# Performance work log

Measured on AMD Instinct MI355X. Metric: run time of the kernel, lower is better.

## Reference

```python
import jax, jax.numpy as jnp
import numpy as np

SPINS = (16, 16)
D_FEAT = 1024
H1 = (4096, 4096, 2048)
H2 = (2048, 1)


def _pair_idx(n):
    # Matches: idx_h1 = [i for i in range(n-1) for j in range(n-1-i)]
    #          h2 = concat(h[k:] for k in 1..n-1)  -> all ordered pairs (i, j), i < j
    i = np.repeat(np.arange(n - 1), np.arange(n - 1, 0, -1))
    j = np.concatenate([np.arange(k + 1, n) for k in range(n - 1)])
    return i.astype(np.int32), j.astype(np.int32)


def setup_inputs():
    key = jax.random.key(0)
    ks = jax.random.split(key, 6)

    def w(k, fi, fo, scale):
        return (scale / np.sqrt(fi)).astype(np.float32) * jax.random.normal(k, (fi, fo), jnp.float32)

    d_in = 2 * D_FEAT
    return {
        "h_one": jax.random.normal(ks[0], (sum(SPINS), D_FEAT), jnp.float32),
        "w1_0": w(ks[1], d_in, H1[0], np.float32(np.sqrt(2.0))),
        "b1_0": jnp.zeros((H1[0],), jnp.float32),
        "w1_1": w(ks[2], H1[0], H1[1], np.float32(np.sqrt(2.0))),
        "b1_1": jnp.zeros((H1[1],), jnp.float32),
        # final mlp1 layer scaled so |hidden| ~ 2: keeps the pair-product finite in fp32
        "w1_2": w(ks[3], H1[1], H1[2], np.float32(2.0)),
        "b1_2": jnp.zeros((H1[2],), jnp.float32),
        "w2_0": w(ks[4], H1[2], H2[0], np.float32(1.0)),
        "b2_0": jnp.zeros((H2[0],), jnp.float32),
        "w2_1": w(ks[5], H2[0], H2[1], np.float32(1.0)),
        "b2_1": jnp.zeros((H2[1],), jnp.float32),
    }


def reference(h_one, w1_0, b1_0, w1_1, b1_1, w1_2, b1_2, w2_0, b2_0, w2_1, b2_1):
    def mlp1(x):  # silu hidden layers, linear output
        x = jax.nn.silu(x @ w1_0 + b1_0)
        x = jax.nn.silu(x @ w1_1 + b1_1)
        return x @ w1_2 + b1_2

    def mlp2(x):  # tanh hidden layer, linear scalar output
        x = jnp.tanh(x @ w2_0 + b2_0)
        return x @ w2_1 + b2_1

    sumlogA = jnp.float32(0.0)
    off = 0
    for n in SPINS:  # fixed, small, structurally distinct loop over spin channels
        h = h_one[off:off + n]
        off += n
        ii, jj = _pair_idx(n)  # static numpy indices
        h1, h2 = h[ii], h[jj]  # [P, D] pairwise gathers, P = n*(n-1)/2
        hidden = mlp1(jnp.concatenate([h1, h2], axis=-1)) \
               - mlp1(jnp.concatenate([h2, h1], axis=-1))  # antisymmetric in (h1, h2)
        a = jnp.prod(hidden, axis=0)  # product-reduce over pairs -> [H1[-1]]
        A = mlp2(a)                   # [1]
        sumlogA = sumlogA + jnp.log(jnp.abs(A)).squeeze()
    return sumlogA
```

## Files before the change

### kernel.cpp

```cpp
#include <hip/hip_runtime.h>
#include <hip/hip_bf16.h>
#include <math.h>


typedef __attribute__((ext_vector_type(8))) short short8;
typedef __attribute__((ext_vector_type(4))) float floatx4;

#define AS1 __attribute__((address_space(1)))
#define AS3 __attribute__((address_space(3)))
#define GLD16(g, l) __builtin_amdgcn_global_load_lds((AS1 const unsigned int*)(g), (AS3 unsigned int*)(l), 16, 0, 0)

__device__ __forceinline__ float silu_f(float x) {
    return x / (1.0f + __expf(-x));
}

__device__ __forceinline__ void split2(float x, unsigned short& hi, unsigned short& lo) {
    unsigned u = __float_as_uint(x);
    unsigned r = u + 0x7FFFu + ((u >> 16) & 1u);
    unsigned short h = (unsigned short)(r >> 16);
    float hf = __uint_as_float((unsigned)h << 16);
    float rem = x - hf;
    unsigned u2 = __float_as_uint(rem);
    unsigned r2 = u2 + 0x7FFFu + ((u2 >> 16) & 1u);
    hi = h;
    lo = (unsigned short)(r2 >> 16);
}

__global__ __launch_bounds__(256)
void transpose_split_all(const float* __restrict__ w10, const float* __restrict__ w11,
                         const float* __restrict__ w12, const float* __restrict__ h_one,
                         unsigned short* __restrict__ t10h, unsigned short* __restrict__ t10l,
                         unsigned short* __restrict__ t11h, unsigned short* __restrict__ t11l,
                         unsigned short* __restrict__ t12h, unsigned short* __restrict__ t12l,
                         unsigned short* __restrict__ Hh, unsigned short* __restrict__ Hl) {
    const int t = threadIdx.x;
    int id = blockIdx.x;

    if (id >= 8192) {
        const int base = (id - 8192) * 4096 + t * 16;
        #pragma unroll
        for (int j = 0; j < 4; ++j) {
            float4 v = *(const float4*)&h_one[base + 4 * j];
            ushort4 hv, lv;
            split2(v.x, hv.x, lv.x);
            split2(v.y, hv.y, lv.y);
            split2(v.z, hv.z, lv.z);
            split2(v.w, hv.w, lv.w);
            *(ushort4*)&Hh[base + 4 * j] = hv;
            *(ushort4*)&Hl[base + 4 * j] = lv;
        }
        return;
    }

    const float* W;
    unsigned short *Th, *Tl;
    int K, N, nt, kt;
    if (id < 2048)       { W = w10; Th = t10h; Tl = t10l; K = 2048; N = 4096; nt = id & 63; kt = id >> 6; }
    else if (id < 6144)  { id -= 2048; W = w11; Th = t11h; Tl = t11l; K = 4096; N = 4096; nt = id & 63; kt = id >> 6; }
    else                 { id -= 6144; W = w12; Th = t12h; Tl = t12l; K = 4096; N = 2048; nt = id & 31; kt = id >> 5; }

    __shared__ float tile[64][65];
    const int n0 = nt * 64;
    const int k0 = kt * 64;

    const int lr = t >> 2;
    const int lc = (t & 3) * 16;
    const float* src = &W[(size_t)(k0 + lr) * N + n0 + lc];
    #pragma unroll
    for (int j = 0; j < 4; ++j) {
        float4 v = *(const float4*)(src + 4 * j);
        tile[lr][lc + 4 * j + 0] = v.x;
        tile[lr][lc + 4 * j + 1] = v.y;
        tile[lr][lc + 4 * j + 2] = v.z;
        tile[lr][lc + 4 * j + 3] = v.w;
    }
    __syncthreads();

    const int sn   = t >> 2;
    const int koff = (t & 3) * 16;
    unsigned short hv[16], lv[16];
    #pragma unroll
    for (int kk = 0; kk < 16; ++kk)
        split2(tile[koff + kk][sn], hv[kk], lv[kk]);
    unsigned short* dh = &Th[(size_t)(n0 + sn) * K + k0 + koff];
    unsigned short* dl = &Tl[(size_t)(n0 + sn) * K + k0 + koff];
    *(short8*)(dh)     = *(short8*)&hv[0];
    *(short8*)(dh + 8) = *(short8*)&hv[8];
    *(short8*)(dl)     = *(short8*)&lv[0];
    *(short8*)(dl + 8) = *(short8*)&lv[8];
}

__global__ __launch_bounds__(256, 2)
void gemm128(const unsigned short* __restrict__ Ah, const unsigned short* __restrict__ Al,
             const unsigned short* __restrict__ Bh, const unsigned short* __restrict__ Bl,
             int K, float* __restrict__ Cpart, int N, int Mtot, int kc)
{
    __shared__ __align__(16) unsigned short As[2][128][32];
    __shared__ __align__(16) unsigned short Bs[2][128][32];

    const int tid  = threadIdx.x;
    const int lane = tid & 63;
    const int wid  = tid >> 6;
    const int n0 = blockIdx.x * 128;
    const int m0 = blockIdx.y * 128;
    const int kbase = blockIdx.z * kc;

    const int srow   = wid * 32 + (lane >> 2);
    const int schunk = (lane & 3) ^ ((srow >> 1) & 3);
    const unsigned short* gA0h = Ah + (size_t)(m0 + srow) * K + kbase + schunk * 8;
    const unsigned short* gA1h = gA0h + (size_t)16 * K;
    const unsigned short* gA0l = Al + (size_t)(m0 + srow) * K + kbase + schunk * 8;
    const unsigned short* gA1l = gA0l + (size_t)16 * K;
    const unsigned short* gB0h = Bh + (size_t)(n0 + srow) * K + kbase + schunk * 8;
    const unsigned short* gB1h = gB0h + (size_t)16 * K;
    const unsigned short* gB0l = Bl + (size_t)(n0 + srow) * K + kbase + schunk * 8;
    const unsigned short* gB1l = gB0l + (size_t)16 * K;
    unsigned short* lA0h = &As[0][wid * 32][0];
    unsigned short* lA1h = &As[0][wid * 32 + 16][0];
    unsigned short* lA0l = &As[1][wid * 32][0];
    unsigned short* lA1l = &As[1][wid * 32 + 16][0];
    unsigned short* lB0h = &Bs[0][wid * 32][0];
    unsigned short* lB1h = &Bs[0][wid * 32 + 16][0];
    unsigned short* lB0l = &Bs[1][wid * 32][0];
    unsigned short* lB1l = &Bs[1][wid * 32 + 16][0];

    const int mhalf = wid >> 1;
    const int nhalf = wid & 1;
    const int lm = lane & 15;
    const int q  = lane >> 4;
    int aoffs[4], boffs[4];
    #pragma unroll
    for (int f = 0; f < 4; ++f) {
        int arow = mhalf * 64 + f * 16 + lm;
        int aslot = q ^ ((arow >> 1) & 3);
        aoffs[f] = arow * 32 + aslot * 8;
        int brow = nhalf * 64 + f * 16 + lm;
        int bslot = q ^ ((brow >> 1) & 3);
        boffs[f] = brow * 32 + bslot * 8;
    }
    const unsigned short* AsF = &As[0][0][0];
    const unsigned short* BsF = &Bs[0][0][0];

    floatx4 acc[4][4];
    #pragma unroll
    for (int ms = 0; ms < 4; ++ms)
        #pragma unroll
        for (int ns = 0; ns < 4; ++ns)
            acc[ms][ns] = (floatx4){0.f, 0.f, 0.f, 0.f};

    const int S = kc >> 5;
    for (int s = 0; s < S; ++s) {
        const int ko = s << 5;
        __syncthreads();
        GLD16(gA0h + ko, lA0h);
        GLD16(gA1h + ko, lA1h);
        GLD16(gA0l + ko, lA0l);
        GLD16(gA1l + ko, lA1l);
        GLD16(gB0h + ko, lB0h);
        GLD16(gB1h + ko, lB1h);
        GLD16(gB0l + ko, lB0l);
        GLD16(gB1l + ko, lB1l);
        __syncthreads();

        short8 afh[4], afl[4], bfh[4], bfl[4];
        #pragma unroll
        for (int f = 0; f < 4; ++f) {
            afh[f] = *(const short8*)(AsF + aoffs[f]);
            afl[f] = *(const short8*)(AsF + 4096 + aoffs[f]);
            bfh[f] = *(const short8*)(BsF + boffs[f]);
            bfl[f] = *(const short8*)(BsF + 4096 + boffs[f]);
        }
        #pragma unroll
        for (int ms = 0; ms < 4; ++ms)
            #pragma unroll
            for (int ns = 0; ns < 4; ++ns)
                acc[ms][ns] = __builtin_amdgcn_mfma_f32_16x16x32_bf16(afh[ms], bfh[ns], acc[ms][ns], 0, 0, 0);
        #pragma unroll
        for (int ms = 0; ms < 4; ++ms)
            #pragma unroll
            for (int ns = 0; ns < 4; ++ns)
                acc[ms][ns] = __builtin_amdgcn_mfma_f32_16x16x32_bf16(afl[ms], bfh[ns], acc[ms][ns], 0, 0, 0);
        #pragma unroll
        for (int ms = 0; ms < 4; ++ms)
            #pragma unroll
            for (int ns = 0; ns < 4; ++ns)
                acc[ms][ns] = __builtin_amdgcn_mfma_f32_16x16x32_bf16(afh[ms], bfl[ns], acc[ms][ns], 0, 0, 0);
    }

    float* Cp = Cpart + (size_t)blockIdx.z * Mtot * N;
    const int lr = (lane >> 4) * 4;
    #pragma unroll
    for (int ms = 0; ms < 4; ++ms)
        #pragma unroll
        for (int ns = 0; ns < 4; ++ns)
            #pragma unroll
            for (int r = 0; r < 4; ++r)
                Cp[(size_t)(m0 + mhalf * 64 + ms * 16 + lr + r) * N + n0 + nhalf * 64 + ns * 16 + lm] = acc[ms][ns][r];
}

__device__ __forceinline__ void load_set(
    const unsigned short* __restrict__ Ah, const unsigned short* __restrict__ Al,
    const unsigned short* __restrict__ Bh, const unsigned short* __restrict__ Bl,
    const unsigned aoff[4], const unsigned boff[4], int koff,
    short8 (&ah)[4], short8 (&al)[4], short8 (&bh)[4], short8 (&bl)[4])
{
    #pragma unroll
    for (int i = 0; i < 4; ++i) {
        ah[i] = *(const short8*)(Ah + aoff[i] + koff);
        al[i] = *(const short8*)(Al + aoff[i] + koff);
        bh[i] = *(const short8*)(Bh + boff[i] + koff);
        bl[i] = *(const short8*)(Bl + boff[i] + koff);
    }
}

__device__ __forceinline__ void mfma_set(
    const short8 (&ah)[4], const short8 (&al)[4],
    const short8 (&bh)[4], const short8 (&bl)[4],
    floatx4 (&acc)[4][4])
{
    #pragma unroll
    for (int ms = 0; ms < 4; ++ms)
        #pragma unroll
        for (int ns = 0; ns < 4; ++ns)
            acc[ms][ns] = __builtin_amdgcn_mfma_f32_16x16x32_bf16(ah[ms], bh[ns], acc[ms][ns], 0, 0, 0);
    #pragma unroll
    for (int ms = 0; ms < 4; ++ms)
        #pragma unroll
        for (int ns = 0; ns < 4; ++ns)
            acc[ms][ns] = __builtin_amdgcn_mfma_f32_16x16x32_bf16(al[ms], bh[ns], acc[ms][ns], 0, 0, 0);
    #pragma unroll
    for (int ms = 0; ms < 4; ++ms)
        #pragma unroll
        for (int ns = 0; ns < 4; ++ns)
            acc[ms][ns] = __builtin_amdgcn_mfma_f32_16x16x32_bf16(ah[ms], bl[ns], acc[ms][ns], 0, 0, 0);
}

__global__ __launch_bounds__(256, 2)
void pq_gemm(const unsigned short* __restrict__ Ah, const unsigned short* __restrict__ Al,
             const unsigned short* __restrict__ Bh0, const unsigned short* __restrict__ Bl0,
             float* __restrict__ PQ)
{
    const int tid  = threadIdx.x;
    const int lane = tid & 63;
    const int wid  = tid >> 6;
    const int n0 = blockIdx.x * 256 + wid * 64;
    const int z  = blockIdx.z;
    const int kbase = (z & 1) * 512;
    const unsigned short* Bh = Bh0 + (z >> 1) * 1024;
    const unsigned short* Bl = Bl0 + (z >> 1) * 1024;
    const int lm = lane & 15;
    const int lk = (lane >> 4) * 8;

    unsigned aoff[4], boff[4];
    #pragma unroll
    for (int i = 0; i < 4; ++i) {
        aoff[i] = (unsigned)(i * 16 + lm) * 1024 + kbase + lk;
        boff[i] = (unsigned)(n0 + i * 16 + lm) * 2048 + kbase + lk;
    }

    floatx4 acc[4][4];
    #pragma unroll
    for (int ms = 0; ms < 4; ++ms)
        #pragma unroll
        for (int ns = 0; ns < 4; ++ns)
            acc[ms][ns] = (floatx4){0.f, 0.f, 0.f, 0.f};

    short8 a0h[4], a0l[4], b0h[4], b0l[4];
    short8 a1h[4], a1l[4], b1h[4], b1l[4];

    load_set(Ah, Al, Bh, Bl, aoff, boff, 0, a0h, a0l, b0h, b0l);
    for (int s = 0; s + 1 < 16; s += 2) {
        load_set(Ah, Al, Bh, Bl, aoff, boff, (s + 1) << 5, a1h, a1l, b1h, b1l);
        mfma_set(a0h, a0l, b0h, b0l, acc);
        if (s + 2 < 16)
            load_set(Ah, Al, Bh, Bl, aoff, boff, (s + 2) << 5, a0h, a0l, b0h, b0l);
        mfma_set(a1h, a1l, b1h, b1l, acc);
    }

    float* Cp = PQ + (size_t)z * 64 * 4096;
    const int lr = (lane >> 4) * 4;
    #pragma unroll
    for (int ms = 0; ms < 4; ++ms)
        #pragma unroll
        for (int ns = 0; ns < 4; ++ns)
            #pragma unroll
            for (int r = 0; r < 4; ++r)
                Cp[(size_t)(ms * 16 + lr + r) * 4096 + n0 + ns * 16 + lm] = acc[ms][ns][r];
}

__global__ __launch_bounds__(256)
void build_y1_kernel(const float* __restrict__ PQ, const float* __restrict__ b1,
                     unsigned short* __restrict__ Y1h, unsigned short* __restrict__ Y1l) {
    const int r = blockIdx.x;
    const int g = r / 240;
    const int rem = r % 240;
    const int o = rem / 120;
    const int p = rem % 120;
    int i = 0, pp = p, cnt = 15;
    while (pp >= cnt) { pp -= cnt; cnt--; i++; }
    const int j = i + 1 + pp;
    const int ai = g * 16 + (o ? j : i);
    const int bi = g * 16 + (o ? i : j);
    const size_t chunk4 = (size_t)64 * 4096 / 4;
    const float4* Pr0 = (const float4*)(PQ + (size_t)ai * 4096);
    const float4* Qr0 = (const float4*)(PQ + (size_t)2 * 64 * 4096 + (size_t)bi * 4096);
    const float4* Br  = (const float4*)b1;
    for (int c = threadIdx.x; c < 1024; c += 256) {
        float4 p0 = Pr0[c], p1 = Pr0[c + chunk4];
        float4 q0 = Qr0[c], q1 = Qr0[c + chunk4];
        float4 bv = Br[c];
        float s0 = silu_f(p0.x + p1.x + q0.x + q1.x + bv.x);
        float s1 = silu_f(p0.y + p1.y + q0.y + q1.y + bv.y);
        float s2 = silu_f(p0.z + p1.z + q0.z + q1.z + bv.z);
        float s3 = silu_f(p0.w + p1.w + q0.w + q1.w + bv.w);
        ushort4 hv, lv;
        split2(s0, hv.x, lv.x);
        split2(s1, hv.y, lv.y);
        split2(s2, hv.z, lv.z);
        split2(s3, hv.w, lv.w);
        *(ushort4*)&Y1h[(size_t)r * 4096 + c * 4] = hv;
        *(ushort4*)&Y1l[(size_t)r * 4096 + c * 4] = lv;
    }
}

__global__ __launch_bounds__(256)
void reduce4_silu_split(const float* __restrict__ Part, const float* __restrict__ bias,
                        unsigned short* __restrict__ Yh, unsigned short* __restrict__ Yl) {
    const size_t idx = (size_t)blockIdx.x * 256 + threadIdx.x;
    const size_t stride4 = (size_t)512 * 4096 / 4;
    const float4* p = (const float4*)Part;
    float4 v0 = p[idx], v1 = p[idx + stride4], v2 = p[idx + 2 * stride4], v3 = p[idx + 3 * stride4];
    const int col = (int)((idx * 4) & 4095);
    float4 b = *(const float4*)&bias[col];
    float s0 = silu_f(v0.x + v1.x + v2.x + v3.x + b.x);
    float s1 = silu_f(v0.y + v1.y + v2.y + v3.y + b.y);
    float s2 = silu_f(v0.z + v1.z + v2.z + v3.z + b.z);
    float s3 = silu_f(v0.w + v1.w + v2.w + v3.w + b.w);
    ushort4 hv, lv;
    split2(s0, hv.x, lv.x);
    split2(s1, hv.y, lv.y);
    split2(s2, hv.z, lv.z);
    split2(s3, hv.w, lv.w);
    *(ushort4*)&Yh[idx * 4] = hv;
    *(ushort4*)&Yl[idx * 4] = lv;
}

__global__ __launch_bounds__(256)
void reduce8_bias(const float* __restrict__ Part, const float* __restrict__ bias,
                  float* __restrict__ Hb) {
    const size_t idx = (size_t)blockIdx.x * 256 + threadIdx.x;
    const size_t stride4 = (size_t)512 * 2048 / 4;
    const float4* p = (const float4*)Part;
    float4 s = p[idx];
    #pragma unroll
    for (int c = 1; c < 8; ++c) {
        float4 v = p[idx + c * stride4];
        s.x += v.x; s.y += v.y; s.z += v.z; s.w += v.w;
    }
    const int col = (int)((idx * 4) & 2047);
    float4 b = *(const float4*)&bias[col];
    s.x += b.x; s.y += b.y; s.z += b.z; s.w += b.w;
    *(float4*)&Hb[idx * 4] = s;
}

__global__ __launch_bounds__(256)
void reduce_prod_kernel(const float* __restrict__ H, float* __restrict__ a_buf) {
    const int g = blockIdx.y;
    const int c = blockIdx.x * 256 + threadIdx.x;
    const float* base = H + (size_t)g * 240 * 2048 + c;
    float prod = 1.0f;
    for (int p = 0; p < 120; ++p) {
        float f = base[(size_t)p * 2048] - base[(size_t)(120 + p) * 2048];
        prod *= f;
    }
    a_buf[g * 2048 + c] = prod;
}

__global__ __launch_bounds__(256)
void mlp2_acc2_kernel(const float* __restrict__ a_buf, const float* __restrict__ W,
                      float* __restrict__ Part2) {
    __shared__ float a0s[256], a1s[256];
    const int kc = blockIdx.y, nc = blockIdx.x, t = threadIdx.x;
    a0s[t] = a_buf[kc * 256 + t];
    a1s[t] = a_buf[2048 + kc * 256 + t];
    __syncthreads();
    const int n = nc * 256 + t;
    const float* Wp = W + (size_t)(kc * 256) * 2048 + n;
    float s0 = 0.f, s1 = 0.f;
    #pragma unroll 8
    for (int kk = 0; kk < 256; ++kk) {
        float w = Wp[(size_t)kk * 2048];
        s0 = fmaf(a0s[kk], w, s0);
        s1 = fmaf(a1s[kk], w, s1);
    }
    Part2[kc * 4096 + n] = s0;
    Part2[kc * 4096 + 2048 + n] = s1;
}

__global__ __launch_bounds__(256)
void finalize_kernel(const float* __restrict__ Part2, const float* __restrict__ b2_0,
                     const float* __restrict__ w2_1, const float* __restrict__ b2_1,
                     float* __restrict__ out) {
    __shared__ float red[256];
    const int tid = threadIdx.x;
    float result = 0.0f;
    for (int g = 0; g < 2; ++g) {
        float s = 0.f;
        for (int n = tid; n < 2048; n += 256) {
            float acc = b2_0[n];
            #pragma unroll
            for (int kc = 0; kc < 8; ++kc)
                acc += Part2[kc * 4096 + g * 2048 + n];
            s += tanhf(acc) * w2_1[n];
        }
        red[tid] = s;
        __syncthreads();
        for (int off = 128; off > 0; off >>= 1) {
            if (tid < off) red[tid] += red[tid + off];
            __syncthreads();
        }
        if (tid == 0) result += logf(fabsf(red[0] + b2_1[0]));
        __syncthreads();
    }
    if (tid == 0) out[0] = result;
}

extern "C" void kernel_launch(void* const* d_in, const int* in_sizes, int n_in,
                              void* d_out, int out_size, void* d_ws, size_t ws_size,
                              hipStream_t stream) {
    const float* h_one = (const float*)d_in[0];
    const float* w1_0  = (const float*)d_in[1];
    const float* b1_0  = (const float*)d_in[2];
    const float* w1_1  = (const float*)d_in[3];
    const float* b1_1  = (const float*)d_in[4];
    const float* w1_2  = (const float*)d_in[5];
    const float* b1_2  = (const float*)d_in[6];
    const float* w2_0  = (const float*)d_in[7];
    const float* b2_0  = (const float*)d_in[8];
    const float* w2_1  = (const float*)d_in[9];
    const float* b2_1  = (const float*)d_in[10];
    float* out = (float*)d_out;

    char* ws = (char*)d_ws;
    unsigned short* W10t_h = (unsigned short*)ws;
    unsigned short* W10t_l = W10t_h + (size_t)4096 * 2048;
    float*          PartL1 = (float*)ws;
    ws += (size_t)4096 * 2048 * 2 * 2;
    unsigned short* W11t_h = (unsigned short*)ws;
    unsigned short* W11t_l = W11t_h + (size_t)4096 * 4096;
    float*          PartL2 = (float*)ws;
    ws += (size_t)4096 * 4096 * 2 * 2;
    unsigned short* W12t_h = (unsigned short*)ws;
    unsigned short* W12t_l = W12t_h + (size_t)2048 * 4096;
    ws += (size_t)2048 * 4096 * 2 * 2;
    unsigned short* Hh  = (unsigned short*)ws;  ws += (size_t)64 * 1024 * 2;
    unsigned short* Hl  = (unsigned short*)ws;  ws += (size_t)64 * 1024 * 2;
    float* PQ  = (float*)ws;                    ws += (size_t)4 * 64 * 4096 * 4;
    unsigned short* Y1h = (unsigned short*)ws;  ws += (size_t)512 * 4096 * 2;
    unsigned short* Y1l = (unsigned short*)ws;  ws += (size_t)512 * 4096 * 2;
    unsigned short* Y2h = (unsigned short*)ws;  ws += (size_t)512 * 4096 * 2;
    unsigned short* Y2l = (unsigned short*)ws;  ws += (size_t)512 * 4096 * 2;
    float* Hb    = (float*)ws;                  ws += (size_t)512 * 2048 * 4;
    float* a_buf = (float*)ws;                  ws += (size_t)2 * 2048 * 4;
    float* Part2 = (float*)ws;                  ws += (size_t)8 * 2 * 2048 * 4;

    transpose_split_all<<<8200, 256, 0, stream>>>(w1_0, w1_1, w1_2, h_one,
                                                  W10t_h, W10t_l, W11t_h, W11t_l,
                                                  W12t_h, W12t_l, Hh, Hl);

    pq_gemm<<<dim3(16, 1, 4), 256, 0, stream>>>(Hh, Hl, W10t_h, W10t_l, PQ);
    build_y1_kernel<<<480, 256, 0, stream>>>(PQ, b1_0, Y1h, Y1l);

    gemm128<<<dim3(32, 4, 4), 256, 0, stream>>>(Y1h, Y1l, W11t_h, W11t_l, 4096,
                                                PartL1, 4096, 512, 1024);
    reduce4_silu_split<<<2048, 256, 0, stream>>>(PartL1, b1_1, Y2h, Y2l);

    gemm128<<<dim3(16, 4, 8), 256, 0, stream>>>(Y2h, Y2l, W12t_h, W12t_l, 4096,
                                                PartL2, 2048, 512, 512);
    reduce8_bias<<<1024, 256, 0, stream>>>(PartL2, b1_2, Hb);

    reduce_prod_kernel<<<dim3(8, 2), 256, 0, stream>>>(Hb, a_buf);
    mlp2_acc2_kernel<<<dim3(8, 8), 256, 0, stream>>>(a_buf, w2_0, Part2);
    finalize_kernel<<<1, 256, 0, stream>>>(Part2, b2_0, w2_1, b2_1, out);
}
```

Before: 380.9 us.

## Restructure weight transpose-split tiles and fuse pair-product into mlp2 kernel

The weight transpose/split kernel now uses 256x32 tiles. Each thread loads a full row segment, splits to bf16 hi/lo before staging in shared memory as 16-bit values, and writes 64-byte contiguous runs of the transposed output. This halves the block count and the shared footprint per element, aiming at better write coalescing. Separately, the product-over-pairs reduction is folded into the mlp2 kernel, removing one launch and the a_buf round trip at the cost of each of 8 column blocks recomputing the same products redundantly.

New measurement: 407.1 us. 1.07x slower.

```diff
diff --git a/kernel.cpp b/kernel.cpp
--- a/kernel.cpp
+++ b/kernel.cpp
@@ -26,6 +26,7 @@
     lo = (unsigned short)(r2 >> 16);
 }
 
+#define TPITCH 264
 __global__ __launch_bounds__(256)
 void transpose_split_all(const float* __restrict__ w10, const float* __restrict__ w11,
                          const float* __restrict__ w12, const float* __restrict__ h_one,
@@ -36,8 +37,8 @@
     const int t = threadIdx.x;
     int id = blockIdx.x;
 
-    if (id >= 8192) {
-        const int base = (id - 8192) * 4096 + t * 16;
+    if (id >= 4096) {
+        const int base = (id - 4096) * 4096 + t * 16;
         #pragma unroll
         for (int j = 0; j < 4; ++j) {
             float4 v = *(const float4*)&h_one[base + 4 * j];
@@ -55,39 +56,41 @@
     const float* W;
     unsigned short *Th, *Tl;
     int K, N, nt, kt;
-    if (id < 2048)       { W = w10; Th = t10h; Tl = t10l; K = 2048; N = 4096; nt = id & 63; kt = id >> 6; }
-    else if (id < 6144)  { id -= 2048; W = w11; Th = t11h; Tl = t11l; K = 4096; N = 4096; nt = id & 63; kt = id >> 6; }
-    else                 { id -= 6144; W = w12; Th = t12h; Tl = t12l; K = 4096; N = 2048; nt = id & 31; kt = id >> 5; }
-
-    __shared__ float tile[64][65];
-    const int n0 = nt * 64;
-    const int k0 = kt * 64;
-
-    const int lr = t >> 2;
-    const int lc = (t & 3) * 16;
-    const float* src = &W[(size_t)(k0 + lr) * N + n0 + lc];
-    #pragma unroll
-    for (int j = 0; j < 4; ++j) {
+    if (id < 1024)       { W = w10; Th = t10h; Tl = t10l; K = 2048; N = 4096; nt = id & 127; kt = id >> 7; }
+    else if (id < 3072)  { id -= 1024; W = w11; Th = t11h; Tl = t11l; K = 4096; N = 4096; nt = id & 127; kt = id >> 7; }
+    else                 { id -= 3072; W = w12; Th = t12h; Tl = t12l; K = 4096; N = 2048; nt = id & 63;  kt = id >> 6; }
+
+    __shared__ unsigned short hs_t[32][TPITCH];
+    __shared__ unsigned short ls_t[32][TPITCH];
+    const int n0 = nt * 32;
+    const int k0 = kt * 256;
+
+    const float* src = &W[(size_t)(k0 + t) * N + n0];
+    #pragma unroll
+    for (int j = 0; j < 8; ++j) {
         float4 v = *(const float4*)(src + 4 * j);
-        tile[lr][lc + 4 * j + 0] = v.x;
-        tile[lr][lc + 4 * j + 1] = v.y;
-        tile[lr][lc + 4 * j + 2] = v.z;
-        tile[lr][lc + 4 * j + 3] = v.w;
+        unsigned short h0, l0, h1, l1, h2, l2, h3, l3;
+        split2(v.x, h0, l0);
+        split2(v.y, h1, l1);
+        split2(v.z, h2, l2);
+        split2(v.w, h3, l3);
+        hs_t[4 * j + 0][t] = h0; ls_t[4 * j + 0][t] = l0;
+        hs_t[4 * j + 1][t] = h1; ls_t[4 * j + 1][t] = l1;
+        hs_t[4 * j + 2][t] = h2; ls_t[4 * j + 2][t] = l2;
+        hs_t[4 * j + 3][t] = h3; ls_t[4 * j + 3][t] = l3;
     }
     __syncthreads();
 
-    const int sn   = t >> 2;
-    const int koff = (t & 3) * 16;
-    unsigned short hv[16], lv[16];
-    #pragma unroll
-    for (int kk = 0; kk < 16; ++kk)
-        split2(tile[koff + kk][sn], hv[kk], lv[kk]);
-    unsigned short* dh = &Th[(size_t)(n0 + sn) * K + k0 + koff];
-    unsigned short* dl = &Tl[(size_t)(n0 + sn) * K + k0 + koff];
-    *(short8*)(dh)     = *(short8*)&hv[0];
-    *(short8*)(dh + 8) = *(short8*)&hv[8];
-    *(short8*)(dl)     = *(short8*)&lv[0];
-    *(short8*)(dl + 8) = *(short8*)&lv[8];
+    const int sn = t >> 3;
+    const int ks = (t & 7) * 32;
+    unsigned short* dh = &Th[(size_t)(n0 + sn) * K + k0 + ks];
+    unsigned short* dl = &Tl[(size_t)(n0 + sn) * K + k0 + ks];
+    #pragma unroll
+    for (int c = 0; c < 4; ++c)
+        *(short8*)(dh + 8 * c) = *(const short8*)&hs_t[sn][ks + 8 * c];
+    #pragma unroll
+    for (int c = 0; c < 4; ++c)
+        *(short8*)(dl + 8 * c) = *(const short8*)&ls_t[sn][ks + 8 * c];
 }
 
 __global__ __launch_bounds__(256, 2)
@@ -364,25 +367,25 @@
 }
 
 __global__ __launch_bounds__(256)
-void reduce_prod_kernel(const float* __restrict__ H, float* __restrict__ a_buf) {
-    const int g = blockIdx.y;
-    const int c = blockIdx.x * 256 + threadIdx.x;
-    const float* base = H + (size_t)g * 240 * 2048 + c;
-    float prod = 1.0f;
-    for (int p = 0; p < 120; ++p) {
-        float f = base[(size_t)p * 2048] - base[(size_t)(120 + p) * 2048];
-        prod *= f;
-    }
-    a_buf[g * 2048 + c] = prod;
-}
-
-__global__ __launch_bounds__(256)
-void mlp2_acc2_kernel(const float* __restrict__ a_buf, const float* __restrict__ W,
-                      float* __restrict__ Part2) {
+void mlp2_fused_kernel(const float* __restrict__ Hb, const float* __restrict__ W,
+                       float* __restrict__ Part2) {
     __shared__ float a0s[256], a1s[256];
     const int kc = blockIdx.y, nc = blockIdx.x, t = threadIdx.x;
-    a0s[t] = a_buf[kc * 256 + t];
-    a1s[t] = a_buf[2048 + kc * 256 + t];
+    const int c = kc * 256 + t;
+    {
+        const float* base0 = Hb + c;
+        const float* base1 = Hb + (size_t)240 * 2048 + c;
+        float pr0 = 1.0f, pr1 = 1.0f;
+        #pragma unroll 4
+        for (int p = 0; p < 120; ++p) {
+            float f0 = base0[(size_t)p * 2048] - base0[(size_t)(120 + p) * 2048];
+            float f1 = base1[(size_t)p * 2048] - base1[(size_t)(120 + p) * 2048];
+            pr0 *= f0;
+            pr1 *= f1;
+        }
+        a0s[t] = pr0;
+        a1s[t] = pr1;
+    }
     __syncthreads();
     const int n = nc * 256 + t;
     const float* Wp = W + (size_t)(kc * 256) * 2048 + n;
@@ -461,10 +464,9 @@
     unsigned short* Y2h = (unsigned short*)ws;  ws += (size_t)512 * 4096 * 2;
     unsigned short* Y2l = (unsigned short*)ws;  ws += (size_t)512 * 4096 * 2;
     float* Hb    = (float*)ws;                  ws += (size_t)512 * 2048 * 4;
-    float* a_buf = (float*)ws;                  ws += (size_t)2 * 2048 * 4;
     float* Part2 = (float*)ws;                  ws += (size_t)8 * 2 * 2048 * 4;
 
-    transpose_split_all<<<8200, 256, 0, stream>>>(w1_0, w1_1, w1_2, h_one,
+    transpose_split_all<<<4104, 256, 0, stream>>>(w1_0, w1_1, w1_2, h_one,
                                                   W10t_h, W10t_l, W11t_h, W11t_l,
                                                   W12t_h, W12t_l, Hh, Hl);
 
@@ -479,7 +481,6 @@
                                                 PartL2, 2048, 512, 512);
     reduce8_bias<<<1024, 256, 0, stream>>>(PartL2, b1_2, Hb);
 
-    reduce_prod_kernel<<<dim3(8, 2), 256, 0, stream>>>(Hb, a_buf);
-    mlp2_acc2_kernel<<<dim3(8, 8), 256, 0, stream>>>(a_buf, w2_0, Part2);
+    mlp2_fused_kernel<<<dim3(8, 8), 256, 0, stream>>>(Hb, w2_0, Part2);
     finalize_kernel<<<1, 256, 0, stream>>>(Part2, b2_0, w2_1, b2_1, out);
 }
```

## Replace first-layer split-bf16 GEMM with direct fp32 vector GEMM and fuse product reduction

Applied to the files above, without the earlier changes.

The first MLP layer no longer transposes and bf16-splits w1_0. A new fp32 FMA kernel reads w1_0 and h_one directly and writes 8 K-chunk partials of the P and Q projections, which build_y1 then sums. This removes one weight transpose pass, the h split and the MFMA pq_gemm launch. The pair product reduction is folded into the mlp2 kernel, which recomputes it in each of its 8 column blocks. gemm128's occupancy hint is raised from 2 to 3 blocks, at the cost of redundant product work and a wider partial reduction in build_y1.

New measurement: 436.8 us. 1.15x slower.

```diff
diff --git a/kernel.cpp b/kernel.cpp
--- a/kernel.cpp
+++ b/kernel.cpp
@@ -27,37 +27,17 @@
 }
 
 __global__ __launch_bounds__(256)
-void transpose_split_all(const float* __restrict__ w10, const float* __restrict__ w11,
-                         const float* __restrict__ w12, const float* __restrict__ h_one,
-                         unsigned short* __restrict__ t10h, unsigned short* __restrict__ t10l,
+void transpose_split_all(const float* __restrict__ w11, const float* __restrict__ w12,
                          unsigned short* __restrict__ t11h, unsigned short* __restrict__ t11l,
-                         unsigned short* __restrict__ t12h, unsigned short* __restrict__ t12l,
-                         unsigned short* __restrict__ Hh, unsigned short* __restrict__ Hl) {
+                         unsigned short* __restrict__ t12h, unsigned short* __restrict__ t12l) {
     const int t = threadIdx.x;
     int id = blockIdx.x;
-
-    if (id >= 8192) {
-        const int base = (id - 8192) * 4096 + t * 16;
-        #pragma unroll
-        for (int j = 0; j < 4; ++j) {
-            float4 v = *(const float4*)&h_one[base + 4 * j];
-            ushort4 hv, lv;
-            split2(v.x, hv.x, lv.x);
-            split2(v.y, hv.y, lv.y);
-            split2(v.z, hv.z, lv.z);
-            split2(v.w, hv.w, lv.w);
-            *(ushort4*)&Hh[base + 4 * j] = hv;
-            *(ushort4*)&Hl[base + 4 * j] = lv;
-        }
-        return;
-    }
 
     const float* W;
     unsigned short *Th, *Tl;
     int K, N, nt, kt;
-    if (id < 2048)       { W = w10; Th = t10h; Tl = t10l; K = 2048; N = 4096; nt = id & 63; kt = id >> 6; }
-    else if (id < 6144)  { id -= 2048; W = w11; Th = t11h; Tl = t11l; K = 4096; N = 4096; nt = id & 63; kt = id >> 6; }
-    else                 { id -= 6144; W = w12; Th = t12h; Tl = t12l; K = 4096; N = 2048; nt = id & 31; kt = id >> 5; }
+    if (id < 4096)  { W = w11; Th = t11h; Tl = t11l; K = 4096; N = 4096; nt = id & 63; kt = id >> 6; }
+    else            { id -= 4096; W = w12; Th = t12h; Tl = t12l; K = 4096; N = 2048; nt = id & 31; kt = id >> 5; }
 
     __shared__ float tile[64][65];
     const int n0 = nt * 64;
@@ -90,7 +70,63 @@
     *(short8*)(dl + 8) = *(short8*)&lv[8];
 }
 
-__global__ __launch_bounds__(256, 2)
+__global__ __launch_bounds__(256)
+void pq_vec(const float* __restrict__ h_one, const float* __restrict__ w10,
+            float* __restrict__ PartPQ) {
+    __shared__ float hs[128][33];
+    const int t  = threadIdx.x;
+    const int nb = blockIdx.x;
+    const int c  = blockIdx.y;
+    const int hcol0 = (c & 7) * 128;
+
+    {
+        const int m   = t >> 3;
+        const int c16 = (t & 7) * 16;
+        const float* src = h_one + (size_t)m * 1024 + hcol0 + c16;
+        #pragma unroll
+        for (int j = 0; j < 4; ++j) {
+            float4 v = *(const float4*)(src + 4 * j);
+            hs[c16 + 4 * j + 0][m] = v.x;
+            hs[c16 + 4 * j + 1][m] = v.y;
+            hs[c16 + 4 * j + 2][m] = v.z;
+            hs[c16 + 4 * j + 3][m] = v.w;
+        }
+    }
+    __syncthreads();
+
+    const int n = nb * 256 + t;
+    const float* Wp = w10 + (size_t)(c * 128) * 4096 + n;
+    float acc[32];
+    #pragma unroll
+    for (int m = 0; m < 32; ++m) acc[m] = 0.f;
+
+    for (int kk = 0; kk < 128; kk += 2) {
+        float w0 = Wp[(size_t)kk * 4096];
+        float w1 = Wp[(size_t)(kk + 1) * 4096];
+        const float4* h0 = (const float4*)&hs[kk][0];
+        const float4* h1 = (const float4*)&hs[kk + 1][0];
+        #pragma unroll
+        for (int m4 = 0; m4 < 8; ++m4) {
+            float4 a = h0[m4];
+            float4 b = h1[m4];
+            acc[4 * m4 + 0] = fmaf(a.x, w0, acc[4 * m4 + 0]);
+            acc[4 * m4 + 1] = fmaf(a.y, w0, acc[4 * m4 + 1]);
+            acc[4 * m4 + 2] = fmaf(a.z, w0, acc[4 * m4 + 2]);
+            acc[4 * m4 + 3] = fmaf(a.w, w0, acc[4 * m4 + 3]);
+            acc[4 * m4 + 0] = fmaf(b.x, w1, acc[4 * m4 + 0]);
+            acc[4 * m4 + 1] = fmaf(b.y, w1, acc[4 * m4 + 1]);
+            acc[4 * m4 + 2] = fmaf(b.z, w1, acc[4 * m4 + 2]);
+            acc[4 * m4 + 3] = fmaf(b.w, w1, acc[4 * m4 + 3]);
+        }
+    }
+
+    float* Cp = PartPQ + (size_t)c * 32 * 4096 + n;
+    #pragma unroll
+    for (int m = 0; m < 32; ++m)
+        Cp[(size_t)m * 4096] = acc[m];
+}
+
+__global__ __launch_bounds__(256, 3)
 void gemm128(const unsigned short* __restrict__ Ah, const unsigned short* __restrict__ Al,
              const unsigned short* __restrict__ Bh, const unsigned short* __restrict__ Bl,
              int K, float* __restrict__ Cpart, int N, int Mtot, int kc)
@@ -198,98 +234,8 @@
                 Cp[(size_t)(m0 + mhalf * 64 + ms * 16 + lr + r) * N + n0 + nhalf * 64 + ns * 16 + lm] = acc[ms][ns][r];
 }
 
-__device__ __forceinline__ void load_set(
-    const unsigned short* __restrict__ Ah, const unsigned short* __restrict__ Al,
-    const unsigned short* __restrict__ Bh, const unsigned short* __restrict__ Bl,
-    const unsigned aoff[4], const unsigned boff[4], int koff,
-    short8 (&ah)[4], short8 (&al)[4], short8 (&bh)[4], short8 (&bl)[4])
-{
-    #pragma unroll
-    for (int i = 0; i < 4; ++i) {
-        ah[i] = *(const short8*)(Ah + aoff[i] + koff);
-        al[i] = *(const short8*)(Al + aoff[i] + koff);
-        bh[i] = *(const short8*)(Bh + boff[i] + koff);
-        bl[i] = *(const short8*)(Bl + boff[i] + koff);
-    }
-}
-
-__device__ __forceinline__ void mfma_set(
-    const short8 (&ah)[4], const short8 (&al)[4],
-    const short8 (&bh)[4], const short8 (&bl)[4],
-    floatx4 (&acc)[4][4])
-{
-    #pragma unroll
-    for (int ms = 0; ms < 4; ++ms)
-        #pragma unroll
-        for (int ns = 0; ns < 4; ++ns)
-            acc[ms][ns] = __builtin_amdgcn_mfma_f32_16x16x32_bf16(ah[ms], bh[ns], acc[ms][ns], 0, 0, 0);
-    #pragma unroll
-    for (int ms = 0; ms < 4; ++ms)
-        #pragma unroll
-        for (int ns = 0; ns < 4; ++ns)
-            acc[ms][ns] = __builtin_amdgcn_mfma_f32_16x16x32_bf16(al[ms], bh[ns], acc[ms][ns], 0, 0, 0);
-    #pragma unroll
-    for (int ms = 0; ms < 4; ++ms)
-        #pragma unroll
-        for (int ns = 0; ns < 4; ++ns)
-            acc[ms][ns] = __builtin_amdgcn_mfma_f32_16x16x32_bf16(ah[ms], bl[ns], acc[ms][ns], 0, 0, 0);
-}
-
-__global__ __launch_bounds__(256, 2)
-void pq_gemm(const unsigned short* __restrict__ Ah, const unsigned short* __restrict__ Al,
-             const unsigned short* __restrict__ Bh0, const unsigned short* __restrict__ Bl0,
-             float* __restrict__ PQ)
-{
-    const int tid  = threadIdx.x;
-    const int lane = tid & 63;
-    const int wid  = tid >> 6;
-    const int n0 = blockIdx.x * 256 + wid * 64;
-    const int z  = blockIdx.z;
-    const int kbase = (z & 1) * 512;
-    const unsigned short* Bh = Bh0 + (z >> 1) * 1024;
-    const unsigned short* Bl = Bl0 + (z >> 1) * 1024;
-    const int lm = lane & 15;
-    const int lk = (lane >> 4) * 8;
-
-    unsigned aoff[4], boff[4];
-    #pragma unroll
-    for (int i = 0; i < 4; ++i) {
-        aoff[i] = (unsigned)(i * 16 + lm) * 1024 + kbase + lk;
-        boff[i] = (unsigned)(n0 + i * 16 + lm) * 2048 + kbase + lk;
-    }
-
-    floatx4 acc[4][4];
-    #pragma unroll
-    for (int ms = 0; ms < 4; ++ms)
-        #pragma unroll
-        for (int ns = 0; ns < 4; ++ns)
-            acc[ms][ns] = (floatx4){0.f, 0.f, 0.f, 0.f};
-
-    short8 a0h[4], a0l[4], b0h[4], b0l[4];
-    short8 a1h[4], a1l[4], b1h[4], b1l[4];
-
-    load_set(Ah, Al, Bh, Bl, aoff, boff, 0, a0h, a0l, b0h, b0l);
-    for (int s = 0; s + 1 < 16; s += 2) {
-        load_set(Ah, Al, Bh, Bl, aoff, boff, (s + 1) << 5, a1h, a1l, b1h, b1l);
-        mfma_set(a0h, a0l, b0h, b0l, acc);
-        if (s + 2 < 16)
-            load_set(Ah, Al, Bh, Bl, aoff, boff, (s + 2) << 5, a0h, a0l, b0h, b0l);
-        mfma_set(a1h, a1l, b1h, b1l, acc);
-    }
-
-    float* Cp = PQ + (size_t)z * 64 * 4096;
-    const int lr = (lane >> 4) * 4;
-    #pragma unroll
-    for (int ms = 0; ms < 4; ++ms)
-        #pragma unroll
-        for (int ns = 0; ns < 4; ++ns)
-            #pragma unroll
-            for (int r = 0; r < 4; ++r)
-                Cp[(size_t)(ms * 16 + lr + r) * 4096 + n0 + ns * 16 + lm] = acc[ms][ns][r];
-}
-
-__global__ __launch_bounds__(256)
-void build_y1_kernel(const float* __restrict__ PQ, const float* __restrict__ b1,
+__global__ __launch_bounds__(256)
+void build_y1_kernel(const float* __restrict__ PartPQ, const float* __restrict__ b1,
                      unsigned short* __restrict__ Y1h, unsigned short* __restrict__ Y1l) {
     const int r = blockIdx.x;
     const int g = r / 240;
@@ -301,18 +247,26 @@
     const int j = i + 1 + pp;
     const int ai = g * 16 + (o ? j : i);
     const int bi = g * 16 + (o ? i : j);
-    const size_t chunk4 = (size_t)64 * 4096 / 4;
-    const float4* Pr0 = (const float4*)(PQ + (size_t)ai * 4096);
-    const float4* Qr0 = (const float4*)(PQ + (size_t)2 * 64 * 4096 + (size_t)bi * 4096);
-    const float4* Br  = (const float4*)b1;
+    const size_t chunk4 = (size_t)32 * 4096 / 4;
+    const float4* Pr = (const float4*)(PartPQ + (size_t)ai * 4096);
+    const float4* Qr = (const float4*)(PartPQ + (size_t)8 * 32 * 4096 + (size_t)bi * 4096);
+    const float4* Br = (const float4*)b1;
     for (int c = threadIdx.x; c < 1024; c += 256) {
-        float4 p0 = Pr0[c], p1 = Pr0[c + chunk4];
-        float4 q0 = Qr0[c], q1 = Qr0[c + chunk4];
+        float sx = 0.f, sy = 0.f, sz = 0.f, sw = 0.f;
+        #pragma unroll
+        for (int ch = 0; ch < 8; ++ch) {
+            float4 pv = Pr[c + ch * chunk4];
+            float4 qv = Qr[c + ch * chunk4];
+            sx += pv.x + qv.x;
+            sy += pv.y + qv.y;
+            sz += pv.z + qv.z;
+            sw += pv.w + qv.w;
+        }
         float4 bv = Br[c];
-        float s0 = silu_f(p0.x + p1.x + q0.x + q1.x + bv.x);
-        float s1 = silu_f(p0.y + p1.y + q0.y + q1.y + bv.y);
-        float s2 = silu_f(p0.z + p1.z + q0.z + q1.z + bv.z);
-        float s3 = silu_f(p0.w + p1.w + q0.w + q1.w + bv.w);
+        float s0 = silu_f(sx + bv.x);
+        float s1 = silu_f(sy + bv.y);
+        float s2 = silu_f(sz + bv.z);
+        float s3 = silu_f(sw + bv.w);
         ushort4 hv, lv;
         split2(s0, hv.x, lv.x);
         split2(s1, hv.y, lv.y);
@@ -364,25 +318,25 @@
 }
 
 __global__ __launch_bounds__(256)
-void reduce_prod_kernel(const float* __restrict__ H, float* __restrict__ a_buf) {
-    const int g = blockIdx.y;
-    const int c = blockIdx.x * 256 + threadIdx.x;
-    const float* base = H + (size_t)g * 240 * 2048 + c;
-    float prod = 1.0f;
-    for (int p = 0; p < 120; ++p) {
-        float f = base[(size_t)p * 2048] - base[(size_t)(120 + p) * 2048];
-        prod *= f;
-    }
-    a_buf[g * 2048 + c] = prod;
-}
-
-__global__ __launch_bounds__(256)
-void mlp2_acc2_kernel(const float* __restrict__ a_buf, const float* __restrict__ W,
-                      float* __restrict__ Part2) {
+void mlp2_fused_kernel(const float* __restrict__ Hb, const float* __restrict__ W,
+                       float* __restrict__ Part2) {
     __shared__ float a0s[256], a1s[256];
     const int kc = blockIdx.y, nc = blockIdx.x, t = threadIdx.x;
-    a0s[t] = a_buf[kc * 256 + t];
-    a1s[t] = a_buf[2048 + kc * 256 + t];
+    const int c = kc * 256 + t;
+    {
+        const float* base0 = Hb + c;
+        const float* base1 = Hb + (size_t)240 * 2048 + c;
+        float pr0 = 1.0f, pr1 = 1.0f;
+        #pragma unroll 4
+        for (int p = 0; p < 120; ++p) {
+            float f0 = base0[(size_t)p * 2048] - base0[(size_t)(120 + p) * 2048];
+            float f1 = base1[(size_t)p * 2048] - base1[(size_t)(120 + p) * 2048];
+            pr0 *= f0;
+            pr1 *= f1;
+        }
+        a0s[t] = pr0;
+        a1s[t] = pr1;
+    }
     __syncthreads();
     const int n = nc * 256 + t;
     const float* Wp = W + (size_t)(kc * 256) * 2048 + n;
@@ -442,10 +396,8 @@
     float* out = (float*)d_out;
 
     char* ws = (char*)d_ws;
-    unsigned short* W10t_h = (unsigned short*)ws;
-    unsigned short* W10t_l = W10t_h + (size_t)4096 * 2048;
-    float*          PartL1 = (float*)ws;
-    ws += (size_t)4096 * 2048 * 2 * 2;
+    float* PartL1 = (float*)ws;
+    ws += (size_t)4 * 512 * 4096 * 4;
     unsigned short* W11t_h = (unsigned short*)ws;
     unsigned short* W11t_l = W11t_h + (size_t)4096 * 4096;
     float*          PartL2 = (float*)ws;
@@ -453,23 +405,20 @@
     unsigned short* W12t_h = (unsigned short*)ws;
     unsigned short* W12t_l = W12t_h + (size_t)2048 * 4096;
     ws += (size_t)2048 * 4096 * 2 * 2;
-    unsigned short* Hh  = (unsigned short*)ws;  ws += (size_t)64 * 1024 * 2;
-    unsigned short* Hl  = (unsigned short*)ws;  ws += (size_t)64 * 1024 * 2;
-    float* PQ  = (float*)ws;                    ws += (size_t)4 * 64 * 4096 * 4;
+    float* PartPQ = (float*)ws;                 ws += (size_t)16 * 32 * 4096 * 4;
     unsigned short* Y1h = (unsigned short*)ws;  ws += (size_t)512 * 4096 * 2;
     unsigned short* Y1l = (unsigned short*)ws;  ws += (size_t)512 * 4096 * 2;
     unsigned short* Y2h = (unsigned short*)ws;  ws += (size_t)512 * 4096 * 2;
     unsigned short* Y2l = (unsigned short*)ws;  ws += (size_t)512 * 4096 * 2;
     float* Hb    = (float*)ws;                  ws += (size_t)512 * 2048 * 4;
-    float* a_buf = (float*)ws;                  ws += (size_t)2 * 2048 * 4;
     float* Part2 = (float*)ws;                  ws += (size_t)8 * 2 * 2048 * 4;
 
-    transpose_split_all<<<8200, 256, 0, stream>>>(w1_0, w1_1, w1_2, h_one,
-                                                  W10t_h, W10t_l, W11t_h, W11t_l,
-                                                  W12t_h, W12t_l, Hh, Hl);
-
-    pq_gemm<<<dim3(16, 1, 4), 256, 0, stream>>>(Hh, Hl, W10t_h, W10t_l, PQ);
-    build_y1_kernel<<<480, 256, 0, stream>>>(PQ, b1_0, Y1h, Y1l);
+    pq_vec<<<dim3(16, 16), 256, 0, stream>>>(h_one, w1_0, PartPQ);
+
+    transpose_split_all<<<6144, 256, 0, stream>>>(w1_1, w1_2,
+                                                  W11t_h, W11t_l, W12t_h, W12t_l);
+
+    build_y1_kernel<<<480, 256, 0, stream>>>(PartPQ, b1_0, Y1h, Y1l);
 
     gemm128<<<dim3(32, 4, 4), 256, 0, stream>>>(Y1h, Y1l, W11t_h, W11t_l, 4096,
                                                 PartL1, 4096, 512, 1024);
@@ -479,7 +428,6 @@
                                                 PartL2, 2048, 512, 512);
     reduce8_bias<<<1024, 256, 0, stream>>>(PartL2, b1_2, Hb);
 
-    reduce_prod_kernel<<<dim3(8, 2), 256, 0, stream>>>(Hb, a_buf);
-    mlp2_acc2_kernel<<<dim3(8, 8), 256, 0, stream>>>(a_buf, w2_0, Part2);
+    mlp2_fused_kernel<<<dim3(8, 8), 256, 0, stream>>>(Hb, w2_0, Part2);
     finalize_kernel<<<1, 256, 0, stream>>>(Part2, b2_0, w2_1, b2_1, out);
 }
```
